# Performance work log

Hardware: AMD Instinct MI355X
Metric: run time of the kernel (lower is better)

The kernel has to match this reference:

```python
import jax, jax.numpy as jnp
import numpy as np

L, D = 6, 2048


def setup_inputs() -> dict:
    key = jax.random.key(0)
    ks = jax.random.split(key, 6)
    # 0.05 scale keeps repeated matrix compositions numerically tame
    W_upper = jax.random.normal(ks[0], (L, D, D), dtype=jnp.float32) * 0.05
    W_lower = jax.random.normal(ks[1], (L, D, D), dtype=jnp.float32) * 0.05
    b_upper = jax.random.normal(ks[2], (L, D), dtype=jnp.float32)
    b_lower = jax.random.normal(ks[3], (L, D), dtype=jnp.float32)
    ub = jax.random.normal(ks[4], (L, D), dtype=jnp.float32)
    lb = jax.random.normal(ks[5], (L, D), dtype=jnp.float32)
    return dict(W_upper=W_upper, W_lower=W_lower, b_upper=b_upper,
                b_lower=b_lower, ub=ub, lb=lb)


def _pos(W):
    # M * W  where M = (W >= 0)
    return jnp.where(W >= 0, W, jnp.zeros_like(W))


def _neg(W):
    # ~M * W where M = (W >= 0)
    return jnp.where(W >= 0, jnp.zeros_like(W), W)


def reference(W_upper, W_lower, b_upper, b_lower, ub, lb):
    # Layer index L-1 is `self`; backsubstitute toward layer 0 (input layer).
    Wu, Wl = W_upper[-1], W_lower[-1]          # [D, D]
    bu, bl = b_upper[-1], b_lower[-1]          # [D]
    best_ub, best_lb = ub[-1], lb[-1]          # [D]
    n_layers = W_upper.shape[0]
    for i in range(n_layers - 2, -1, -1):      # prev = layer i
        Wu_p, Wu_n = _pos(Wu), _neg(Wu)
        Wl_p, Wl_n = _pos(Wl), _neg(Wl)
        # concrete bounds through prev's pre-activation bounds
        cur_ub = Wu_p @ ub[i] + Wu_n @ lb[i] + bu
        cur_lb = Wl_p @ lb[i] + Wl_n @ ub[i] + bl
        best_ub = jnp.minimum(best_ub, cur_ub)
        best_lb = jnp.maximum(best_lb, cur_lb)
        # compose symbolic bounds with prev layer's relaxation
        bu = Wu_p @ b_upper[i] + Wu_n @ b_lower[i] + bu
        bl = Wl_p @ b_lower[i] + Wl_n @ b_upper[i] + bl
        Wu = Wu_p @ W_upper[i] + Wu_n @ W_lower[i]
        Wl = Wl_p @ W_lower[i] + Wl_n @ W_upper[i]
    # final concretization against the input layer's bounds (layer 0)
    Wu_p, Wu_n = _pos(Wu), _neg(Wu)
    Wl_p, Wl_n = _pos(Wl), _neg(Wl)
    cur_ub = Wu_p @ ub[0] + Wu_n @ lb[0] + bu
    cur_lb = Wl_p @ lb[0] + Wl_n @ ub[0] + bl
    best_ub = jnp.minimum(best_ub, cur_ub)
    best_lb = jnp.maximum(best_lb, cur_lb)
    return best_ub, best_lb
```

## Files before the change

### kernel.cpp

```cpp
#include <hip/hip_runtime.h>

#define D 2048
#define DD ((size_t)D * (size_t)D)

typedef __attribute__((ext_vector_type(8))) short bf16x8;
typedef __attribute__((ext_vector_type(16))) float f32x16;

#define GLOBAL_AS __attribute__((address_space(1)))
#define LDS_AS __attribute__((address_space(3)))

__device__ inline unsigned short f2bf(float f) {
  unsigned u = __float_as_uint(f);
  u += 0x7fffu + ((u >> 16) & 1u);
  return (unsigned short)(u >> 16);
}
__device__ inline float bf2f(unsigned us) {
  return __uint_as_float(us << 16);
}

__global__ void init_vecs(const float* __restrict__ b_upper5,
                          const float* __restrict__ b_lower5,
                          const float* __restrict__ ub5,
                          const float* __restrict__ lb5,
                          float* __restrict__ bu, float* __restrict__ bl,
                          float* __restrict__ out) {
  int t = blockIdx.x * blockDim.x + threadIdx.x;
  if (t < D) {
    bu[t] = b_upper5[t];
    bl[t] = b_lower5[t];
    out[t] = ub5[t];
    out[D + t] = lb5[t];
  }
}

__global__ __launch_bounds__(256) void prep(
    const float* __restrict__ Wu32, const float* __restrict__ Wl32,
    const unsigned short* __restrict__ WuA, const unsigned short* __restrict__ WlA,
    const float* __restrict__ ubi, const float* __restrict__ lbi,
    const float* __restrict__ bupi, const float* __restrict__ bloi,
    float* __restrict__ bu, float* __restrict__ bl,
    float* __restrict__ best,
    unsigned short* __restrict__ oU, unsigned short* __restrict__ oL,
    const float* __restrict__ Wup, const float* __restrict__ Wlo,
    unsigned short* __restrict__ BsT, unsigned short* __restrict__ BdT,
    int update_bias, int first) {
  __shared__ float red[4][4];
  __shared__ unsigned short sS[64][68];
  __shared__ unsigned short sD[64][68];

  const int t = threadIdx.x;

  if (blockIdx.x < 2048) {
    const int r = blockIdx.x;
    const size_t base = (size_t)r * D + t * 8;
    const int c = t * 8;

    float wu[8], wl[8];
    if (first) {
      float4 wu0 = *(const float4*)(Wu32 + base), wu1 = *(const float4*)(Wu32 + base + 4);
      float4 wl0 = *(const float4*)(Wl32 + base), wl1 = *(const float4*)(Wl32 + base + 4);
      wu[0] = wu0.x; wu[1] = wu0.y; wu[2] = wu0.z; wu[3] = wu0.w;
      wu[4] = wu1.x; wu[5] = wu1.y; wu[6] = wu1.z; wu[7] = wu1.w;
      wl[0] = wl0.x; wl[1] = wl0.y; wl[2] = wl0.z; wl[3] = wl0.w;
      wl[4] = wl1.x; wl[5] = wl1.y; wl[6] = wl1.z; wl[7] = wl1.w;
      uint4 w;
      w.x = f2bf(wu[0]) | ((unsigned)f2bf(wu[1]) << 16);
      w.y = f2bf(wu[2]) | ((unsigned)f2bf(wu[3]) << 16);
      w.z = f2bf(wu[4]) | ((unsigned)f2bf(wu[5]) << 16);
      w.w = f2bf(wu[6]) | ((unsigned)f2bf(wu[7]) << 16);
      *(uint4*)(oU + base) = w;
      w.x = f2bf(wl[0]) | ((unsigned)f2bf(wl[1]) << 16);
      w.y = f2bf(wl[2]) | ((unsigned)f2bf(wl[3]) << 16);
      w.z = f2bf(wl[4]) | ((unsigned)f2bf(wl[5]) << 16);
      w.w = f2bf(wl[6]) | ((unsigned)f2bf(wl[7]) << 16);
      *(uint4*)(oL + base) = w;
    } else {
      uint4 a = *(const uint4*)(WuA + base);
      uint4 b = *(const uint4*)(WlA + base);
      wu[0] = bf2f(a.x & 0xffffu); wu[1] = bf2f(a.x >> 16);
      wu[2] = bf2f(a.y & 0xffffu); wu[3] = bf2f(a.y >> 16);
      wu[4] = bf2f(a.z & 0xffffu); wu[5] = bf2f(a.z >> 16);
      wu[6] = bf2f(a.w & 0xffffu); wu[7] = bf2f(a.w >> 16);
      wl[0] = bf2f(b.x & 0xffffu); wl[1] = bf2f(b.x >> 16);
      wl[2] = bf2f(b.y & 0xffffu); wl[3] = bf2f(b.y >> 16);
      wl[4] = bf2f(b.z & 0xffffu); wl[5] = bf2f(b.z >> 16);
      wl[6] = bf2f(b.w & 0xffffu); wl[7] = bf2f(b.w >> 16);
    }

    float4 u0 = *(const float4*)(ubi + c),  u1 = *(const float4*)(ubi + c + 4);
    float4 l0 = *(const float4*)(lbi + c),  l1 = *(const float4*)(lbi + c + 4);
    float4 p0 = *(const float4*)(bupi + c), p1 = *(const float4*)(bupi + c + 4);
    float4 n0 = *(const float4*)(bloi + c), n1 = *(const float4*)(bloi + c + 4);
    float uu[8] = {u0.x, u0.y, u0.z, u0.w, u1.x, u1.y, u1.z, u1.w};
    float ll[8] = {l0.x, l0.y, l0.z, l0.w, l1.x, l1.y, l1.z, l1.w};
    float pp[8] = {p0.x, p0.y, p0.z, p0.w, p1.x, p1.y, p1.z, p1.w};
    float nn[8] = {n0.x, n0.y, n0.z, n0.w, n1.x, n1.y, n1.z, n1.w};

    float su_c = 0.f, su_b = 0.f, sl_c = 0.f, sl_b = 0.f;
    #pragma unroll
    for (int j = 0; j < 8; ++j) {
      su_c += wu[j] * (wu[j] >= 0.f ? uu[j] : ll[j]);
      su_b += wu[j] * (wu[j] >= 0.f ? pp[j] : nn[j]);
      sl_c += wl[j] * (wl[j] >= 0.f ? ll[j] : uu[j]);
      sl_b += wl[j] * (wl[j] >= 0.f ? nn[j] : pp[j]);
    }

    #pragma unroll
    for (int off = 32; off; off >>= 1) {
      su_c += __shfl_down(su_c, off);
      su_b += __shfl_down(su_b, off);
      sl_c += __shfl_down(sl_c, off);
      sl_b += __shfl_down(sl_b, off);
    }
    int wave = t >> 6;
    if ((t & 63) == 0) {
      red[0][wave] = su_c; red[1][wave] = su_b;
      red[2][wave] = sl_c; red[3][wave] = sl_b;
    }
    __syncthreads();
    if (t == 0) {
      float a = red[0][0] + red[0][1] + red[0][2] + red[0][3];
      float b = red[1][0] + red[1][1] + red[1][2] + red[1][3];
      float cc = red[2][0] + red[2][1] + red[2][2] + red[2][3];
      float d = red[3][0] + red[3][1] + red[3][2] + red[3][3];
      float bu_old = bu[r], bl_old = bl[r];
      best[r]     = fminf(best[r],     a + bu_old);
      best[D + r] = fmaxf(best[D + r], cc + bl_old);
      if (update_bias) {
        bu[r] = b + bu_old;
        bl[r] = d + bl_old;
      }
    }
  } else {
    const int bx = blockIdx.x - 2048;
    const int k0 = (bx >> 5) * 64, c0 = (bx & 31) * 64;
    const int tx = t & 15, ty = t >> 4;
    #pragma unroll
    for (int r = 0; r < 4; ++r) {
      int kk = ty + r * 16;
      size_t g = (size_t)(k0 + kk) * D + c0 + tx * 4;
      float4 up = *(const float4*)(Wup + g);
      float4 lo = *(const float4*)(Wlo + g);
      sS[kk][tx * 4 + 0] = f2bf((up.x + lo.x) * 0.5f);
      sS[kk][tx * 4 + 1] = f2bf((up.y + lo.y) * 0.5f);
      sS[kk][tx * 4 + 2] = f2bf((up.z + lo.z) * 0.5f);
      sS[kk][tx * 4 + 3] = f2bf((up.w + lo.w) * 0.5f);
      sD[kk][tx * 4 + 0] = f2bf((up.x - lo.x) * 0.5f);
      sD[kk][tx * 4 + 1] = f2bf((up.y - lo.y) * 0.5f);
      sD[kk][tx * 4 + 2] = f2bf((up.z - lo.z) * 0.5f);
      sD[kk][tx * 4 + 3] = f2bf((up.w - lo.w) * 0.5f);
    }
    __syncthreads();
    #pragma unroll
    for (int r = 0; r < 4; ++r) {
      int cc = ty + r * 16;
      int kq = tx * 4;
      unsigned a0 = sS[kq + 0][cc] | ((unsigned)sS[kq + 1][cc] << 16);
      unsigned a1 = sS[kq + 2][cc] | ((unsigned)sS[kq + 3][cc] << 16);
      *(uint2*)(BsT + (size_t)(c0 + cc) * D + k0 + kq) = make_uint2(a0, a1);
      a0 = sD[kq + 0][cc] | ((unsigned)sD[kq + 1][cc] << 16);
      a1 = sD[kq + 2][cc] | ((unsigned)sD[kq + 3][cc] << 16);
      *(uint2*)(BdT + (size_t)(c0 + cc) * D + k0 + kq) = make_uint2(a0, a1);
    }
  }
}

__global__ __launch_bounds__(512, 2) void gemm_fused(
    const unsigned short* __restrict__ w16U,
    const unsigned short* __restrict__ w16L,
    const unsigned short* __restrict__ BsT,
    const unsigned short* __restrict__ BdT,
    unsigned short* __restrict__ Cu, unsigned short* __restrict__ Cl) {
  extern __shared__ unsigned char lds[];

  const int bid = blockIdx.x;
  const int vid = (bid & 7) * 32 + (bid >> 3);
  const int row0 = (vid >> 4) * 128, col0 = (vid & 15) * 128;

  const int tid = threadIdx.x;
  const int lane = tid & 63, wid = tid >> 6;
  const int grp = wid >> 2;
  const int w2 = wid & 3;
  const int wr = w2 >> 1, wc = w2 & 1;
  const int l31 = lane & 31, kh = lane >> 5;

  const int srow8 = lane >> 3;
  const int slot  = lane & 7;
  int rowc[2], swel[2];
  #pragma unroll
  for (int c = 0; c < 2; ++c) {
    rowc[c] = (wid + c * 8) * 8 + srow8;
    swel[c] = (slot ^ (rowc[c] & 7)) * 8;
  }
  const unsigned short* gAU[2]; const unsigned short* gAL[2];
  const unsigned short* gBs[2]; const unsigned short* gBd[2];
  #pragma unroll
  for (int c = 0; c < 2; ++c) {
    gAU[c] = w16U + (size_t)(row0 + rowc[c]) * D + swel[c];
    gAL[c] = w16L + (size_t)(row0 + rowc[c]) * D + swel[c];
    gBs[c] = BsT + (size_t)(col0 + rowc[c]) * D + swel[c];
    gBd[c] = BdT + (size_t)(col0 + rowc[c]) * D + swel[c];
  }

  f32x16 acc[2][2] = {};

  int aoff[2][4], boff[2][4];
  #pragma unroll
  for (int mb = 0; mb < 2; ++mb) {
    int ar = wr * 64 + mb * 32 + l31;
    #pragma unroll
    for (int ks = 0; ks < 4; ++ks)
      aoff[mb][ks] = ar * 128 + (((ks * 2 + kh) ^ (ar & 7)) * 16);
  }
  #pragma unroll
  for (int nb = 0; nb < 2; ++nb) {
    int bc = wc * 64 + nb * 32 + l31;
    #pragma unroll
    for (int ks = 0; ks < 4; ++ks)
      boff[nb][ks] = bc * 128 + (((ks * 2 + kh) ^ (bc & 7)) * 16);
  }

  #define STAGE(curb, kt)                                                          \
    do {                                                                           \
      unsigned bb = (unsigned)(curb) * 65536u;                                     \
      _Pragma("unroll")                                                            \
      for (int c = 0; c < 2; ++c) {                                                \
        unsigned dst = bb + (unsigned)(wid + c * 8) * 1024u;                       \
        __builtin_amdgcn_global_load_lds((const GLOBAL_AS unsigned*)(gAU[c] + (kt)),\
            (LDS_AS unsigned*)(lds + 0 + dst), 16, 0, 0);                          \
        __builtin_amdgcn_global_load_lds((const GLOBAL_AS unsigned*)(gAL[c] + (kt)),\
            (LDS_AS unsigned*)(lds + 16384 + dst), 16, 0, 0);                      \
        __builtin_amdgcn_global_load_lds((const GLOBAL_AS unsigned*)(gBs[c] + (kt)),\
            (LDS_AS unsigned*)(lds + 32768 + dst), 16, 0, 0);                      \
        __builtin_amdgcn_global_load_lds((const GLOBAL_AS unsigned*)(gBd[c] + (kt)),\
            (LDS_AS unsigned*)(lds + 49152 + dst), 16, 0, 0);                      \
      }                                                                            \
    } while (0)

  STAGE(0, 0);
  __syncthreads();

  int cur = 0;
  const unsigned Abase = grp ? 16384u : 0u;
  for (int t = 0; t < 32; ++t) {
    if (t < 31) STAGE(cur ^ 1, (t + 1) * 64);

    const unsigned char* Ab = lds + Abase + cur * 65536;
    const unsigned char* Sb = lds + 32768 + cur * 65536;
    const unsigned char* Db = lds + 49152 + cur * 65536;

    #pragma unroll
    for (int ks = 0; ks < 4; ++ks) {
      bf16x8 aw0 = *(const bf16x8*)(Ab + aoff[0][ks]);
      bf16x8 aw1 = *(const bf16x8*)(Ab + aoff[1][ks]);
      bf16x8 bs0 = *(const bf16x8*)(Sb + boff[0][ks]);
      bf16x8 bs1 = *(const bf16x8*)(Sb + boff[1][ks]);
      bf16x8 bd0 = *(const bf16x8*)(Db + boff[0][ks]);
      bf16x8 bd1 = *(const bf16x8*)(Db + boff[1][ks]);
      if (grp) { bd0 ^= (short)0x8000; bd1 ^= (short)0x8000; }
      bf16x8 av0 = aw0 & (short)0x7fff;
      bf16x8 av1 = aw1 & (short)0x7fff;

      acc[0][0] = __builtin_amdgcn_mfma_f32_32x32x16_bf16(aw0, bs0, acc[0][0], 0, 0, 0);
      acc[0][0] = __builtin_amdgcn_mfma_f32_32x32x16_bf16(av0, bd0, acc[0][0], 0, 0, 0);
      acc[0][1] = __builtin_amdgcn_mfma_f32_32x32x16_bf16(aw0, bs1, acc[0][1], 0, 0, 0);
      acc[0][1] = __builtin_amdgcn_mfma_f32_32x32x16_bf16(av0, bd1, acc[0][1], 0, 0, 0);
      acc[1][0] = __builtin_amdgcn_mfma_f32_32x32x16_bf16(aw1, bs0, acc[1][0], 0, 0, 0);
      acc[1][0] = __builtin_amdgcn_mfma_f32_32x32x16_bf16(av1, bd0, acc[1][0], 0, 0, 0);
      acc[1][1] = __builtin_amdgcn_mfma_f32_32x32x16_bf16(aw1, bs1, acc[1][1], 0, 0, 0);
      acc[1][1] = __builtin_amdgcn_mfma_f32_32x32x16_bf16(av1, bd1, acc[1][1], 0, 0, 0);
    }

    __syncthreads();
    cur ^= 1;
  }
  #undef STAGE

  unsigned short* C = grp ? Cl : Cu;
  #pragma unroll
  for (int mb = 0; mb < 2; ++mb)
    #pragma unroll
    for (int nb = 0; nb < 2; ++nb) {
      const int colg = col0 + wc * 64 + nb * 32 + l31;
      const int rowb = row0 + wr * 64 + mb * 32 + kh * 4;
      #pragma unroll
      for (int g = 0; g < 4; ++g)
        #pragma unroll
        for (int j = 0; j < 4; ++j)
          C[(size_t)(rowb + g * 8 + j) * D + colg] = f2bf(acc[mb][nb][g * 4 + j]);
    }
}

extern "C" void kernel_launch(void* const* d_in, const int* in_sizes, int n_in,
                              void* d_out, int out_size, void* d_ws, size_t ws_size,
                              hipStream_t stream) {
  const float* W_upper = (const float*)d_in[0];
  const float* W_lower = (const float*)d_in[1];
  const float* b_upper = (const float*)d_in[2];
  const float* b_lower = (const float*)d_in[3];
  const float* ub      = (const float*)d_in[4];
  const float* lb      = (const float*)d_in[5];
  float* out = (float*)d_out;

  unsigned short* aU[2]; unsigned short* aL[2];
  aU[0] = (unsigned short*)d_ws;
  aL[0] = aU[0] + DD;
  aU[1] = aL[0] + DD;
  aL[1] = aU[1] + DD;
  unsigned short* BsT = aL[1] + DD;
  unsigned short* BdT = BsT + DD;
  float* bu = (float*)(BdT + DD);
  float* bl = bu + D;

  static_cast<void>(hipFuncSetAttribute(
      (const void*)gemm_fused, hipFuncAttributeMaxDynamicSharedMemorySize, 131072));

  init_vecs<<<(D + 255) / 256, 256, 0, stream>>>(
      b_upper + 5 * D, b_lower + 5 * D, ub + 5 * D, lb + 5 * D, bu, bl, out);

  int cur = 0;
  for (int i = 4; i >= 0; --i) {
    const int first = (i == 4);
    prep<<<3072, 256, 0, stream>>>(
        W_upper + 5 * DD, W_lower + 5 * DD,
        aU[cur], aL[cur],
        ub + (size_t)i * D, lb + (size_t)i * D,
        b_upper + (size_t)i * D, b_lower + (size_t)i * D,
        bu, bl, out,
        aU[cur], aL[cur],
        W_upper + (size_t)i * DD, W_lower + (size_t)i * DD,
        BsT, BdT, 1, first);
    gemm_fused<<<256, 512, 131072, stream>>>(aU[cur], aL[cur], BsT, BdT,
                                             aU[cur ^ 1], aL[cur ^ 1]);
    cur ^= 1;
  }
  prep<<<2048, 256, 0, stream>>>(
      (const float*)nullptr, (const float*)nullptr,
      aU[cur], aL[cur],
      ub, lb, b_upper, b_lower, bu, bl, out,
      (unsigned short*)nullptr, (unsigned short*)nullptr,
      (const float*)nullptr, (const float*)nullptr,
      (unsigned short*)nullptr, (unsigned short*)nullptr, 0, 0);
}
```

Baseline: 439.2 us.

## Split K across wave halves instead of upper/lower outputs, reduce through LDS

```diff
diff --git a/kernel.cpp b/kernel.cpp
--- a/kernel.cpp
+++ b/kernel.cpp
@@ -179,7 +179,7 @@
 
   const int tid = threadIdx.x;
   const int lane = tid & 63, wid = tid >> 6;
-  const int grp = wid >> 2;
+  const int h = wid >> 2;
   const int w2 = wid & 3;
   const int wr = w2 >> 1, wc = w2 & 1;
   const int l31 = lane & 31, kh = lane >> 5;
@@ -202,22 +202,22 @@
     gBd[c] = BdT + (size_t)(col0 + rowc[c]) * D + swel[c];
   }
 
-  f32x16 acc[2][2] = {};
-
-  int aoff[2][4], boff[2][4];
+  f32x16 acc[2][2][2] = {};
+
+  int aoff[2][2], boff[2][2];
   #pragma unroll
   for (int mb = 0; mb < 2; ++mb) {
     int ar = wr * 64 + mb * 32 + l31;
     #pragma unroll
-    for (int ks = 0; ks < 4; ++ks)
-      aoff[mb][ks] = ar * 128 + (((ks * 2 + kh) ^ (ar & 7)) * 16);
+    for (int ksl = 0; ksl < 2; ++ksl)
+      aoff[mb][ksl] = ar * 128 + ((((h * 2 + ksl) * 2 + kh) ^ (ar & 7)) * 16);
   }
   #pragma unroll
   for (int nb = 0; nb < 2; ++nb) {
     int bc = wc * 64 + nb * 32 + l31;
     #pragma unroll
-    for (int ks = 0; ks < 4; ++ks)
-      boff[nb][ks] = bc * 128 + (((ks * 2 + kh) ^ (bc & 7)) * 16);
+    for (int ksl = 0; ksl < 2; ++ksl)
+      boff[nb][ksl] = bc * 128 + ((((h * 2 + ksl) * 2 + kh) ^ (bc & 7)) * 16);
   }
 
   #define STAGE(curb, kt)                                                          \
@@ -241,34 +241,46 @@
   __syncthreads();
 
   int cur = 0;
-  const unsigned Abase = grp ? 16384u : 0u;
   for (int t = 0; t < 32; ++t) {
     if (t < 31) STAGE(cur ^ 1, (t + 1) * 64);
 
-    const unsigned char* Ab = lds + Abase + cur * 65536;
+    const unsigned char* Ub = lds + 0 + cur * 65536;
+    const unsigned char* Lb = lds + 16384 + cur * 65536;
     const unsigned char* Sb = lds + 32768 + cur * 65536;
     const unsigned char* Db = lds + 49152 + cur * 65536;
 
     #pragma unroll
-    for (int ks = 0; ks < 4; ++ks) {
-      bf16x8 aw0 = *(const bf16x8*)(Ab + aoff[0][ks]);
-      bf16x8 aw1 = *(const bf16x8*)(Ab + aoff[1][ks]);
-      bf16x8 bs0 = *(const bf16x8*)(Sb + boff[0][ks]);
-      bf16x8 bs1 = *(const bf16x8*)(Sb + boff[1][ks]);
-      bf16x8 bd0 = *(const bf16x8*)(Db + boff[0][ks]);
-      bf16x8 bd1 = *(const bf16x8*)(Db + boff[1][ks]);
-      if (grp) { bd0 ^= (short)0x8000; bd1 ^= (short)0x8000; }
-      bf16x8 av0 = aw0 & (short)0x7fff;
-      bf16x8 av1 = aw1 & (short)0x7fff;
-
-      acc[0][0] = __builtin_amdgcn_mfma_f32_32x32x16_bf16(aw0, bs0, acc[0][0], 0, 0, 0);
-      acc[0][0] = __builtin_amdgcn_mfma_f32_32x32x16_bf16(av0, bd0, acc[0][0], 0, 0, 0);
-      acc[0][1] = __builtin_amdgcn_mfma_f32_32x32x16_bf16(aw0, bs1, acc[0][1], 0, 0, 0);
-      acc[0][1] = __builtin_amdgcn_mfma_f32_32x32x16_bf16(av0, bd1, acc[0][1], 0, 0, 0);
-      acc[1][0] = __builtin_amdgcn_mfma_f32_32x32x16_bf16(aw1, bs0, acc[1][0], 0, 0, 0);
-      acc[1][0] = __builtin_amdgcn_mfma_f32_32x32x16_bf16(av1, bd0, acc[1][0], 0, 0, 0);
-      acc[1][1] = __builtin_amdgcn_mfma_f32_32x32x16_bf16(aw1, bs1, acc[1][1], 0, 0, 0);
-      acc[1][1] = __builtin_amdgcn_mfma_f32_32x32x16_bf16(av1, bd1, acc[1][1], 0, 0, 0);
+    for (int ksl = 0; ksl < 2; ++ksl) {
+      bf16x8 au0 = *(const bf16x8*)(Ub + aoff[0][ksl]);
+      bf16x8 au1 = *(const bf16x8*)(Ub + aoff[1][ksl]);
+      bf16x8 al0 = *(const bf16x8*)(Lb + aoff[0][ksl]);
+      bf16x8 al1 = *(const bf16x8*)(Lb + aoff[1][ksl]);
+      bf16x8 bs0 = *(const bf16x8*)(Sb + boff[0][ksl]);
+      bf16x8 bs1 = *(const bf16x8*)(Sb + boff[1][ksl]);
+      bf16x8 bd0 = *(const bf16x8*)(Db + boff[0][ksl]);
+      bf16x8 bd1 = *(const bf16x8*)(Db + boff[1][ksl]);
+
+      bf16x8 vu0 = au0 & (short)0x7fff;
+      bf16x8 vu1 = au1 & (short)0x7fff;
+      bf16x8 vl0 = al0 | (short)0x8000;
+      bf16x8 vl1 = al1 | (short)0x8000;
+
+      acc[0][0][0] = __builtin_amdgcn_mfma_f32_32x32x16_bf16(au0, bs0, acc[0][0][0], 0, 0, 0);
+      acc[0][0][0] = __builtin_amdgcn_mfma_f32_32x32x16_bf16(vu0, bd0, acc[0][0][0], 0, 0, 0);
+      acc[0][0][1] = __builtin_amdgcn_mfma_f32_32x32x16_bf16(au0, bs1, acc[0][0][1], 0, 0, 0);
+      acc[0][0][1] = __builtin_amdgcn_mfma_f32_32x32x16_bf16(vu0, bd1, acc[0][0][1], 0, 0, 0);
+      acc[0][1][0] = __builtin_amdgcn_mfma_f32_32x32x16_bf16(au1, bs0, acc[0][1][0], 0, 0, 0);
+      acc[0][1][0] = __builtin_amdgcn_mfma_f32_32x32x16_bf16(vu1, bd0, acc[0][1][0], 0, 0, 0);
+      acc[0][1][1] = __builtin_amdgcn_mfma_f32_32x32x16_bf16(au1, bs1, acc[0][1][1], 0, 0, 0);
+      acc[0][1][1] = __builtin_amdgcn_mfma_f32_32x32x16_bf16(vu1, bd1, acc[0][1][1], 0, 0, 0);
+      acc[1][0][0] = __builtin_amdgcn_mfma_f32_32x32x16_bf16(al0, bs0, acc[1][0][0], 0, 0, 0);
+      acc[1][0][0] = __builtin_amdgcn_mfma_f32_32x32x16_bf16(vl0, bd0, acc[1][0][0], 0, 0, 0);
+      acc[1][0][1] = __builtin_amdgcn_mfma_f32_32x32x16_bf16(al0, bs1, acc[1][0][1], 0, 0, 0);
+      acc[1][0][1] = __builtin_amdgcn_mfma_f32_32x32x16_bf16(vl0, bd1, acc[1][0][1], 0, 0, 0);
+      acc[1][1][0] = __builtin_amdgcn_mfma_f32_32x32x16_bf16(al1, bs0, acc[1][1][0], 0, 0, 0);
+      acc[1][1][0] = __builtin_amdgcn_mfma_f32_32x32x16_bf16(vl1, bd0, acc[1][1][0], 0, 0, 0);
+      acc[1][1][1] = __builtin_amdgcn_mfma_f32_32x32x16_bf16(al1, bs1, acc[1][1][1], 0, 0, 0);
+      acc[1][1][1] = __builtin_amdgcn_mfma_f32_32x32x16_bf16(vl1, bd1, acc[1][1][1], 0, 0, 0);
     }
 
     __syncthreads();
@@ -276,19 +288,39 @@
   }
   #undef STAGE
 
-  unsigned short* C = grp ? Cl : Cu;
-  #pragma unroll
-  for (int mb = 0; mb < 2; ++mb)
-    #pragma unroll
-    for (int nb = 0; nb < 2; ++nb) {
-      const int colg = col0 + wc * 64 + nb * 32 + l31;
-      const int rowb = row0 + wr * 64 + mb * 32 + kh * 4;
+  const unsigned rbase = (unsigned)w2 * 32768u + (unsigned)lane * 64u;
+  if (h == 1) {
+    #pragma unroll
+    for (int u = 0; u < 2; ++u)
       #pragma unroll
-      for (int g = 0; g < 4; ++g)
+      for (int mb = 0; mb < 2; ++mb)
         #pragma unroll
-        for (int j = 0; j < 4; ++j)
-          C[(size_t)(rowb + g * 8 + j) * D + colg] = f2bf(acc[mb][nb][g * 4 + j]);
-    }
+        for (int nb = 0; nb < 2; ++nb)
+          *(f32x16*)(lds + rbase + (unsigned)(((u * 2 + mb) * 2 + nb)) * 4096u)
+              = acc[u][mb][nb];
+  }
+  __syncthreads();
+  if (h == 0) {
+    #pragma unroll
+    for (int u = 0; u < 2; ++u) {
+      unsigned short* C = u ? Cl : Cu;
+      #pragma unroll
+      for (int mb = 0; mb < 2; ++mb)
+        #pragma unroll
+        for (int nb = 0; nb < 2; ++nb) {
+          f32x16 p = *(const f32x16*)(lds + rbase +
+                       (unsigned)(((u * 2 + mb) * 2 + nb)) * 4096u);
+          f32x16 s = acc[u][mb][nb] + p;
+          const int colg = col0 + wc * 64 + nb * 32 + l31;
+          const int rowb = row0 + wr * 64 + mb * 32 + kh * 4;
+          #pragma unroll
+          for (int g = 0; g < 4; ++g)
+            #pragma unroll
+            for (int j = 0; j < 4; ++j)
+              C[(size_t)(rowb + g * 8 + j) * D + colg] = f2bf(s[g * 4 + j]);
+        }
+    }
+  }
 }
 
 extern "C" void kernel_launch(void* const* d_in, const int* in_sizes, int n_in,
```

Measured after the change: 422.3 us, median of 2. 1.04x faster.
